# Optimization experiments

Measured on AMD Instinct MI355X. Metric: run time of the kernel, lower is better.

Reference implementation:

```python
import jax, jax.numpy as jnp
import numpy as np

N_USERS = 200000
N_ITEMS = 100000
N = N_USERS + N_ITEMS
DIM = 64
N_EDGES = 9600000
N_LAYERS = 3
BATCH = 16384


def setup_inputs() -> dict:
    key = jax.random.key(0)
    k = jax.random.split(key, 7)
    user_emb = 0.01 * jax.random.normal(k[0], (N_USERS, DIM), dtype=jnp.float32)
    item_emb = 0.01 * jax.random.normal(k[1], (N_ITEMS, DIM), dtype=jnp.float32)
    rows = jax.random.randint(k[2], (N_EDGES,), 0, N, dtype=jnp.int64)
    cols = jax.random.randint(k[3], (N_EDGES,), 0, N, dtype=jnp.int64)
    # normalized-adjacency-like positive values
    vals = jax.random.uniform(k[4], (N_EDGES,), dtype=jnp.float32) * 0.01
    U = jax.random.randint(k[5], (BATCH,), 0, N_USERS, dtype=jnp.int64)
    I = jax.random.randint(k[6], (BATCH,), 0, N_ITEMS, dtype=jnp.int64)
    return {"user_emb": user_emb, "item_emb": item_emb, "vals": vals,
            "rows": rows, "cols": cols, "U": U, "I": I}


def _spmm(rows, cols, vals, E):
    # A_hat @ E for COO A_hat: gather source rows, scale, scatter-add to dest rows
    msgs = vals[:, None] * E[cols]                      # [nnz, d]
    return jax.ops.segment_sum(msgs, rows, num_segments=N)


def reference(user_emb, item_emb, vals, rows, cols, U, I):
    E = jnp.concatenate([user_emb, item_emb], axis=0)   # [N, d]
    acc = E
    for _ in range(N_LAYERS):
        E = _spmm(rows, cols, vals, E)
        acc = acc + E
    out = acc / (N_LAYERS + 1)                          # mean over layer stack
    E_u = out[:N_USERS]
    E_i = out[N_USERS:]
    return (E_u[U] * E_i[I]).sum(-1)                    # [BATCH]
```

## Files before the change

kernel.cpp:

```cpp
#include <hip/hip_runtime.h>

#define N_USERS 200000
#define N_ITEMS 100000
#define NN      300000
#define DIM     64
#define N_EDGES 9600000
#define BATCH   16384
#define BSH2    10
#define NB2     293
#define CHUNK2  4096
#define CAP     34304

__device__ __forceinline__ unsigned short f2bf(float f) {
    unsigned b = __float_as_uint(f);
    return (unsigned short)((b + 0x7FFF + ((b >> 16) & 1)) >> 16);
}
__device__ __forceinline__ float bf2f(unsigned short u) {
    return __uint_as_float((unsigned)u << 16);
}

__global__ void to_bf16(const float* __restrict__ ue, const float* __restrict__ ie,
                        unsigned short* __restrict__ E) {
    const size_t nU = (size_t)N_USERS * DIM / 4;
    const size_t nT = (size_t)NN * DIM / 4;
    const float4* u4 = (const float4*)ue;
    const float4* i4 = (const float4*)ie;
    ushort4* E4 = (ushort4*)E;
    size_t stride = (size_t)gridDim.x * blockDim.x;
    for (size_t k = (size_t)blockIdx.x * blockDim.x + threadIdx.x; k < nT; k += stride) {
        float4 v = (k < nU) ? u4[k] : i4[k - nU];
        ushort4 o;
        o.x = f2bf(v.x); o.y = f2bf(v.y); o.z = f2bf(v.z); o.w = f2bf(v.w);
        E4[k] = o;
    }
}

__global__ __launch_bounds__(256) void bin_sort(const int* __restrict__ rows,
                                                const int* __restrict__ cols,
                                                const float* __restrict__ vals,
                                                int* __restrict__ gfill,
                                                int2* __restrict__ estage) {
    __shared__ int  hist[NB2 + 1];
    __shared__ int  sc[NB2 + 1];
    __shared__ int  gbase[NB2];
    __shared__ int  rankc[NB2];
    __shared__ int2 st[CHUNK2];

    int tid = threadIdx.x;
    int e0 = blockIdx.x * CHUNK2;
    int e1 = min(e0 + CHUNK2, N_EDGES);
    int n  = e1 - e0;

    for (int i = tid; i <= NB2; i += 256) { hist[i] = 0; sc[i] = 0; }
    __syncthreads();

    for (int e = e0 + tid; e < e1; e += 256)
        atomicAdd(&hist[rows[e] >> BSH2], 1);
    __syncthreads();

    for (int i = tid; i < NB2; i += 256) sc[i] = hist[i];
    __syncthreads();

    for (int off = 1; off < NB2; off <<= 1) {
        int i0 = tid, i1 = tid + 256;
        int a0 = 0, a1 = 0;
        if (i0 < NB2 && i0 >= off) a0 = sc[i0 - off];
        if (i1 < NB2 && i1 >= off) a1 = sc[i1 - off];
        __syncthreads();
        if (i0 < NB2 && i0 >= off) sc[i0] += a0;
        if (i1 < NB2 && i1 >= off) sc[i1] += a1;
        __syncthreads();
    }

    for (int b = tid; b < NB2; b += 256) {
        int cb = hist[b];
        hist[b] = sc[b] - cb;
        gbase[b] = b * CAP + (cb ? atomicAdd(&gfill[b], cb) : 0);
        rankc[b] = 0;
    }
    if (tid == 0) hist[NB2] = CHUNK2 + 1;
    __syncthreads();

    for (int e = e0 + tid; e < e1; e += 256) {
        int r = rows[e];
        int c = cols[e];
        float v = vals[e];
        int b = r >> BSH2;
        int lr = atomicAdd(&rankc[b], 1);
        st[hist[b] + lr] = make_int2(((r & 1023) << 19) | c, __float_as_int(v));
    }
    __syncthreads();

    for (int i = tid; i < n; i += 256) {
        int lo = 0, hi = NB2;
        while (hi - lo > 1) {
            int mid = (lo + hi) >> 1;
            if (hist[mid] <= i) lo = mid; else hi = mid;
        }
        estage[gbase[lo] + (i - hist[lo])] = st[i];
    }
}

__global__ __launch_bounds__(1024) void row_scatter(const int* __restrict__ gfill,
                                                    const int2* __restrict__ estage,
                                                    int2* __restrict__ epack,
                                                    int* __restrict__ rp) {
    __shared__ int lcnt[1024];
    __shared__ int s[1024];
    int b = blockIdx.x;
    int r0 = b << BSH2;
    int nr = min(1024, NN - r0);
    int tid = threadIdx.x;
    lcnt[tid] = 0;
    __syncthreads();

    int ebeg = b * CAP;
    int cnt  = gfill[b];
    for (int e = tid; e < cnt; e += 1024)
        atomicAdd(&lcnt[((unsigned)estage[ebeg + e].x) >> 19], 1);
    __syncthreads();

    int x = lcnt[tid];
    s[tid] = x;
    __syncthreads();
    for (int off = 1; off < 1024; off <<= 1) {
        int t = (tid >= off) ? s[tid - off] : 0;
        __syncthreads();
        s[tid] += t;
        __syncthreads();
    }
    int myptr = ebeg + s[tid] - x;
    if (tid < nr) rp[r0 + b + tid] = myptr;
    if (tid == 0) rp[r0 + b + nr] = ebeg + cnt;
    lcnt[tid] = myptr;
    __syncthreads();

    for (int e = tid; e < cnt; e += 1024) {
        int2 ed = estage[ebeg + e];
        int rl = ((unsigned)ed.x) >> 19;
        int pos = atomicAdd(&lcnt[rl], 1);
        epack[pos] = make_int2(ed.x & 0x7FFFF, ed.y);
    }
}

__device__ __forceinline__ float row_dot(const int2* __restrict__ ep, int beg, int end,
                                         const unsigned short* __restrict__ E, int lane) {
    const long long* epl = (const long long*)ep;
    float acc = 0.f;
    int j = beg;
    int jend8 = beg + ((end - beg) & ~7);
    for (; j < jend8; j += 8) {
        long long d[8];
        #pragma unroll
        for (int k = 0; k < 8; ++k) d[k] = __builtin_nontemporal_load(&epl[j + k]);
        float x[8];
        #pragma unroll
        for (int k = 0; k < 8; ++k)
            x[k] = bf2f(E[(size_t)(int)(d[k] & 0x7FFFF) * DIM + lane]);
        #pragma unroll
        for (int k = 0; k < 8; ++k)
            acc = __builtin_fmaf(__int_as_float((int)(d[k] >> 32)), x[k], acc);
    }
    if (j + 4 <= end) {
        long long d[4];
        #pragma unroll
        for (int k = 0; k < 4; ++k) d[k] = __builtin_nontemporal_load(&epl[j + k]);
        float x[4];
        #pragma unroll
        for (int k = 0; k < 4; ++k)
            x[k] = bf2f(E[(size_t)(int)(d[k] & 0x7FFFF) * DIM + lane]);
        #pragma unroll
        for (int k = 0; k < 4; ++k)
            acc = __builtin_fmaf(__int_as_float((int)(d[k] >> 32)), x[k], acc);
        j += 4;
    }
    for (; j < end; ++j) {
        long long d = __builtin_nontemporal_load(&epl[j]);
        acc = __builtin_fmaf(__int_as_float((int)(d >> 32)),
                             bf2f(E[(size_t)(int)(d & 0x7FFFF) * DIM + lane]), acc);
    }
    return acc;
}

__global__ void spmm_csr(const int* __restrict__ rp, const int2* __restrict__ ep,
                         const unsigned short* __restrict__ Ein,
                         unsigned short* __restrict__ Eout) {
    int lane = threadIdx.x & 63;
    int w = (int)((blockIdx.x * (size_t)blockDim.x + threadIdx.x) >> 6);
    int row = __builtin_amdgcn_readfirstlane(w);
    if (row >= NN) return;
    int idx = row + (row >> BSH2);
    int beg = rp[idx];
    int end = rp[idx + 1];
    float acc = row_dot(ep, beg, end, Ein, lane);
    __builtin_nontemporal_store(f2bf(acc), &Eout[(size_t)row * DIM + lane]);
}

__global__ void spmm_target(const int* __restrict__ rp, const int2* __restrict__ ep,
                            const unsigned short* __restrict__ Ein,
                            const int* __restrict__ U, const int* __restrict__ I,
                            float* __restrict__ accU, float* __restrict__ accI) {
    int lane = threadIdx.x & 63;
    int w = (int)((blockIdx.x * (size_t)blockDim.x + threadIdx.x) >> 6);
    if (w >= 2 * BATCH) return;
    int row;
    float* accp;
    if (w < BATCH) { row = U[w];                   accp = accU + (size_t)w * DIM; }
    else           { row = N_USERS + I[w - BATCH]; accp = accI + (size_t)(w - BATCH) * DIM; }
    row = __builtin_amdgcn_readfirstlane(row);
    int idx = row + (row >> BSH2);
    int beg = rp[idx];
    int end = rp[idx + 1];
    float acc = row_dot(ep, beg, end, Ein, lane);
    accp[lane] += acc;
}

__global__ void acc_init(const float* __restrict__ ue, const float* __restrict__ ie,
                         const int* __restrict__ U, const int* __restrict__ I,
                         float* __restrict__ accU, float* __restrict__ accI) {
    int t = blockIdx.x * blockDim.x + threadIdx.x;
    int b = t >> 6, d = t & 63;
    accU[t] = ue[(size_t)U[b] * DIM + d];
    accI[t] = ie[(size_t)I[b] * DIM + d];
}

__global__ void acc_add(const unsigned short* __restrict__ E, const int* __restrict__ U,
                        const int* __restrict__ I, float* __restrict__ accU,
                        float* __restrict__ accI) {
    int t = blockIdx.x * blockDim.x + threadIdx.x;
    int b = t >> 6, d = t & 63;
    accU[t] += bf2f(E[(size_t)U[b] * DIM + d]);
    accI[t] += bf2f(E[(size_t)(N_USERS + I[b]) * DIM + d]);
}

__global__ void dot_out(const float* __restrict__ accU, const float* __restrict__ accI,
                        float* __restrict__ out) {
    int t = blockIdx.x * blockDim.x + threadIdx.x;
    int b = t >> 6, lane = threadIdx.x & 63;
    float p = accU[t] * accI[t];
    #pragma unroll
    for (int off = 32; off; off >>= 1) p += __shfl_xor(p, off, 64);
    if (lane == 0) out[b] = p * (1.0f / 16.0f);
}

extern "C" void kernel_launch(void* const* d_in, const int* in_sizes, int n_in,
                              void* d_out, int out_size, void* d_ws, size_t ws_size,
                              hipStream_t stream) {
    const float* ue   = (const float*)d_in[0];
    const float* ie   = (const float*)d_in[1];
    const float* vals = (const float*)d_in[2];
    const int*   rows = (const int*)d_in[3];
    const int*   cols = (const int*)d_in[4];
    const int*   U    = (const int*)d_in[5];
    const int*   I    = (const int*)d_in[6];
    float* out = (float*)d_out;

    char* ws = (char*)d_ws;
    const size_t EPbytes = (size_t)NB2 * CAP * sizeof(int2);
    const size_t EBbytes = (size_t)NN * DIM * sizeof(unsigned short);
    const size_t ACbytes = (size_t)BATCH * DIM * sizeof(float);
    const size_t RPbytes = ((size_t)(NN + NB2 + 1) * sizeof(int) + 255) & ~(size_t)255;
    const size_t NBbytes = (((size_t)(NB2 + 1) * sizeof(int)) + 255) & ~(size_t)255;

    size_t off = 0;
    int2*  epack  = (int2*)(ws + off);                   off += EPbytes;
    char*  region2 = ws + off;                           off += EPbytes;
    float* accU   = (float*)(ws + off); off += ACbytes;
    float* accI   = (float*)(ws + off); off += ACbytes;
    int*   rp     = (int*)(ws + off);   off += RPbytes;
    int*   gfill  = (int*)(ws + off);   off += NBbytes;

    int2* estage = (int2*)region2;
    unsigned short* Ebf_a = (unsigned short*)region2;
    unsigned short* Ebf_b = (unsigned short*)(region2 + EBbytes);

    const int nBinBlocks = (N_EDGES + CHUNK2 - 1) / CHUNK2;

    hipMemsetAsync(gfill, 0, (size_t)(NB2 + 1) * sizeof(int), stream);
    bin_sort<<<nBinBlocks, 256, 0, stream>>>(rows, cols, vals, gfill, estage);
    row_scatter<<<NB2, 1024, 0, stream>>>(gfill, estage, epack, rp);

    to_bf16<<<2048, 256, 0, stream>>>(ue, ie, Ebf_a);
    acc_init<<<BATCH * DIM / 256, 256, 0, stream>>>(ue, ie, U, I, accU, accI);

    const int spmmBlocks = (NN * 64 + 255) / 256;

    spmm_csr<<<spmmBlocks, 256, 0, stream>>>(rp, epack, Ebf_a, Ebf_b);
    acc_add<<<BATCH * DIM / 256, 256, 0, stream>>>(Ebf_b, U, I, accU, accI);

    spmm_csr<<<spmmBlocks, 256, 0, stream>>>(rp, epack, Ebf_b, Ebf_a);
    acc_add<<<BATCH * DIM / 256, 256, 0, stream>>>(Ebf_a, U, I, accU, accI);

    spmm_target<<<2 * BATCH * 64 / 256, 256, 0, stream>>>(rp, epack, Ebf_a, U, I, accU, accI);

    dot_out<<<BATCH / 4, 256, 0, stream>>>(accU, accI, out);
}
```

Baseline: 697.7 us.

## Shrink row buckets to 256 rows and stage bucket edges in LDS

The COO-to-CSR build now uses 1172 buckets of 256 rows instead of 293 buckets of 1024. Each row_scatter block copies its whole bucket (up to 9216 edges) into shared memory once, then runs the count and scatter passes from LDS instead of reading the global staging buffer twice. The trade-off is a larger histogram and scan in bin_sort, about 72KB of LDS per row_scatter block (which limits occupancy), and a smaller per-bucket capacity margin.

```diff
diff --git a/kernel.cpp b/kernel.cpp
--- a/kernel.cpp
+++ b/kernel.cpp
@@ -6,10 +6,10 @@
 #define DIM     64
 #define N_EDGES 9600000
 #define BATCH   16384
-#define BSH2    10
-#define NB2     293
+#define BSH3    8
+#define NBK     1172
 #define CHUNK2  4096
-#define CAP     34304
+#define CAP3    9216
 
 __device__ __forceinline__ unsigned short f2bf(float f) {
     unsigned b = __float_as_uint(f);
@@ -40,10 +40,10 @@
                                                 const float* __restrict__ vals,
                                                 int* __restrict__ gfill,
                                                 int2* __restrict__ estage) {
-    __shared__ int  hist[NB2 + 1];
-    __shared__ int  sc[NB2 + 1];
-    __shared__ int  gbase[NB2];
-    __shared__ int  rankc[NB2];
+    __shared__ int  hist[NBK + 1];
+    __shared__ int  sc[NBK];
+    __shared__ int  gbase[NBK];
+    __shared__ int  rankc[NBK];
     __shared__ int2 st[CHUNK2];
 
     int tid = threadIdx.x;
@@ -51,48 +51,53 @@
     int e1 = min(e0 + CHUNK2, N_EDGES);
     int n  = e1 - e0;
 
-    for (int i = tid; i <= NB2; i += 256) { hist[i] = 0; sc[i] = 0; }
+    for (int i = tid; i <= NBK; i += 256) hist[i] = 0;
     __syncthreads();
 
     for (int e = e0 + tid; e < e1; e += 256)
-        atomicAdd(&hist[rows[e] >> BSH2], 1);
-    __syncthreads();
-
-    for (int i = tid; i < NB2; i += 256) sc[i] = hist[i];
-    __syncthreads();
-
-    for (int off = 1; off < NB2; off <<= 1) {
-        int i0 = tid, i1 = tid + 256;
-        int a0 = 0, a1 = 0;
-        if (i0 < NB2 && i0 >= off) a0 = sc[i0 - off];
-        if (i1 < NB2 && i1 >= off) a1 = sc[i1 - off];
+        atomicAdd(&hist[rows[e] >> BSH3], 1);
+    __syncthreads();
+
+    for (int i = tid; i < NBK; i += 256) sc[i] = hist[i];
+    __syncthreads();
+
+    for (int off = 1; off < NBK; off <<= 1) {
+        int a[5];
+        #pragma unroll
+        for (int k = 0; k < 5; ++k) {
+            int i = tid + (k << 8);
+            a[k] = (i < NBK && i >= off) ? sc[i - off] : 0;
+        }
         __syncthreads();
-        if (i0 < NB2 && i0 >= off) sc[i0] += a0;
-        if (i1 < NB2 && i1 >= off) sc[i1] += a1;
+        #pragma unroll
+        for (int k = 0; k < 5; ++k) {
+            int i = tid + (k << 8);
+            if (i < NBK && i >= off) sc[i] += a[k];
+        }
         __syncthreads();
     }
 
-    for (int b = tid; b < NB2; b += 256) {
+    for (int b = tid; b < NBK; b += 256) {
         int cb = hist[b];
         hist[b] = sc[b] - cb;
-        gbase[b] = b * CAP + (cb ? atomicAdd(&gfill[b], cb) : 0);
+        gbase[b] = b * CAP3 + (cb ? atomicAdd(&gfill[b], cb) : 0);
         rankc[b] = 0;
     }
-    if (tid == 0) hist[NB2] = CHUNK2 + 1;
+    if (tid == 0) hist[NBK] = CHUNK2 + 1;
     __syncthreads();
 
     for (int e = e0 + tid; e < e1; e += 256) {
         int r = rows[e];
         int c = cols[e];
         float v = vals[e];
-        int b = r >> BSH2;
+        int b = r >> BSH3;
         int lr = atomicAdd(&rankc[b], 1);
-        st[hist[b] + lr] = make_int2(((r & 1023) << 19) | c, __float_as_int(v));
+        st[hist[b] + lr] = make_int2(((r & 255) << 19) | c, __float_as_int(v));
     }
     __syncthreads();
 
     for (int i = tid; i < n; i += 256) {
-        int lo = 0, hi = NB2;
+        int lo = 0, hi = NBK;
         while (hi - lo > 1) {
             int mid = (lo + hi) >> 1;
             if (hist[mid] <= i) lo = mid; else hi = mid;
@@ -105,38 +110,41 @@
                                                     const int2* __restrict__ estage,
                                                     int2* __restrict__ epack,
                                                     int* __restrict__ rp) {
-    __shared__ int lcnt[1024];
-    __shared__ int s[1024];
+    __shared__ int2 st[CAP3];
+    __shared__ int  lcnt[256];
+    __shared__ int  s[256];
     int b = blockIdx.x;
-    int r0 = b << BSH2;
-    int nr = min(1024, NN - r0);
+    int r0 = b << BSH3;
+    int nr = min(256, NN - r0);
     int tid = threadIdx.x;
-    lcnt[tid] = 0;
-    __syncthreads();
-
-    int ebeg = b * CAP;
+    int ebeg = b * CAP3;
     int cnt  = gfill[b];
+
+    for (int e = tid; e < cnt; e += 1024) st[e] = estage[ebeg + e];
+    if (tid < 256) lcnt[tid] = 0;
+    __syncthreads();
+
     for (int e = tid; e < cnt; e += 1024)
-        atomicAdd(&lcnt[((unsigned)estage[ebeg + e].x) >> 19], 1);
-    __syncthreads();
-
-    int x = lcnt[tid];
-    s[tid] = x;
-    __syncthreads();
-    for (int off = 1; off < 1024; off <<= 1) {
-        int t = (tid >= off) ? s[tid - off] : 0;
+        atomicAdd(&lcnt[((unsigned)st[e].x) >> 19], 1);
+    __syncthreads();
+
+    int x = 0;
+    if (tid < 256) { x = lcnt[tid]; s[tid] = x; }
+    __syncthreads();
+    for (int off = 1; off < 256; off <<= 1) {
+        int t = 0;
+        if (tid < 256 && tid >= off) t = s[tid - off];
         __syncthreads();
-        s[tid] += t;
+        if (tid < 256 && tid >= off) s[tid] += t;
         __syncthreads();
     }
-    int myptr = ebeg + s[tid] - x;
-    if (tid < nr) rp[r0 + b + tid] = myptr;
+    if (tid < nr) rp[r0 + b + tid] = ebeg + s[tid] - x;
     if (tid == 0) rp[r0 + b + nr] = ebeg + cnt;
-    lcnt[tid] = myptr;
+    if (tid < 256) lcnt[tid] = ebeg + s[tid] - x;
     __syncthreads();
 
     for (int e = tid; e < cnt; e += 1024) {
-        int2 ed = estage[ebeg + e];
+        int2 ed = st[e];
         int rl = ((unsigned)ed.x) >> 19;
         int pos = atomicAdd(&lcnt[rl], 1);
         epack[pos] = make_int2(ed.x & 0x7FFFF, ed.y);
@@ -189,7 +197,7 @@
     int w = (int)((blockIdx.x * (size_t)blockDim.x + threadIdx.x) >> 6);
     int row = __builtin_amdgcn_readfirstlane(w);
     if (row >= NN) return;
-    int idx = row + (row >> BSH2);
+    int idx = row + (row >> BSH3);
     int beg = rp[idx];
     int end = rp[idx + 1];
     float acc = row_dot(ep, beg, end, Ein, lane);
@@ -208,7 +216,7 @@
     if (w < BATCH) { row = U[w];                   accp = accU + (size_t)w * DIM; }
     else           { row = N_USERS + I[w - BATCH]; accp = accI + (size_t)(w - BATCH) * DIM; }
     row = __builtin_amdgcn_readfirstlane(row);
-    int idx = row + (row >> BSH2);
+    int idx = row + (row >> BSH3);
     int beg = rp[idx];
     int end = rp[idx + 1];
     float acc = row_dot(ep, beg, end, Ein, lane);
@@ -256,11 +264,11 @@
     float* out = (float*)d_out;
 
     char* ws = (char*)d_ws;
-    const size_t EPbytes = (size_t)NB2 * CAP * sizeof(int2);
+    const size_t EPbytes = (size_t)NBK * CAP3 * sizeof(int2);
     const size_t EBbytes = (size_t)NN * DIM * sizeof(unsigned short);
     const size_t ACbytes = (size_t)BATCH * DIM * sizeof(float);
-    const size_t RPbytes = ((size_t)(NN + NB2 + 1) * sizeof(int) + 255) & ~(size_t)255;
-    const size_t NBbytes = (((size_t)(NB2 + 1) * sizeof(int)) + 255) & ~(size_t)255;
+    const size_t RPbytes = ((size_t)(NN + NBK + 1) * sizeof(int) + 255) & ~(size_t)255;
+    const size_t NBbytes = (((size_t)(NBK + 1) * sizeof(int)) + 255) & ~(size_t)255;
 
     size_t off = 0;
     int2*  epack  = (int2*)(ws + off);                   off += EPbytes;
@@ -276,9 +284,9 @@
 
     const int nBinBlocks = (N_EDGES + CHUNK2 - 1) / CHUNK2;
 
-    hipMemsetAsync(gfill, 0, (size_t)(NB2 + 1) * sizeof(int), stream);
+    hipMemsetAsync(gfill, 0, (size_t)(NBK + 1) * sizeof(int), stream);
     bin_sort<<<nBinBlocks, 256, 0, stream>>>(rows, cols, vals, gfill, estage);
-    row_scatter<<<NB2, 1024, 0, stream>>>(gfill, estage, epack, rp);
+    row_scatter<<<NBK, 1024, 0, stream>>>(gfill, estage, epack, rp);
 
     to_bf16<<<2048, 256, 0, stream>>>(ue, ie, Ebf_a);
     acc_init<<<BATCH * DIM / 256, 256, 0, stream>>>(ue, ie, U, I, accU, accI);
```

New measurement: 693.6 us. Within noise of the previous version (-0.6%).
